# Performance work log

Hardware: AMD Instinct MI355X
Metric: run time of the kernel (lower is better)

Reference implementation:

```python
import jax, jax.numpy as jnp
import numpy as np

N, E = 50000, 1600000
NODE_F, EDGE_F = 128, 64
H, F = 4, 16
NEG_SLOPE = 0.2


def setup_inputs() -> dict:
    key = jax.random.key(0)
    ks = jax.random.split(key, 12)
    return {
        "nfeat": jax.random.normal(ks[0], (N, NODE_F), jnp.float32),
        "efeat": jax.random.normal(ks[1], (E, EDGE_F), jnp.float32),
        "W_node": jax.random.normal(ks[2], (NODE_F, H * F), jnp.float32) * 0.1,
        "b_node": jax.random.normal(ks[3], (H * F,), jnp.float32) * 0.1,
        "W_edge": jax.random.normal(ks[4], (EDGE_F, H * F), jnp.float32) * 0.1,
        "b_edge": jax.random.normal(ks[5], (H * F,), jnp.float32) * 0.1,
        "attn_l": jax.random.normal(ks[6], (H, F), jnp.float32) * 0.1,
        "attn_r": jax.random.normal(ks[7], (H, F), jnp.float32) * 0.1,
        "attn_e": jax.random.normal(ks[8], (H, F), jnp.float32) * 0.1,
        "src": jax.random.randint(ks[9], (E,), 0, N, jnp.int32),
        "dst": jax.random.randint(ks[10], (E,), 0, N, jnp.int32),
    }


def reference(nfeat, efeat, W_node, b_node, W_edge, b_edge,
              attn_l, attn_r, attn_e, src, dst):
    n = nfeat.shape[0]
    node_feat = (nfeat @ W_node + b_node).reshape(n, H, F)   # [N,H,F]
    edge_feat = (efeat @ W_edge + b_edge).reshape(-1, H, F)  # [E,H,F]
    el = jnp.einsum('nhf,hf->nh', node_feat, attn_l)  # [N,H]
    er = jnp.einsum('nhf,hf->nh', node_feat, attn_r)  # [N,H]
    ee = jnp.einsum('ehf,hf->eh', edge_feat, attn_e)  # [E,H]
    el_prime = el[src] + ee                            # u_add_e, [E,H]
    e = el_prime + er[dst]                             # e_add_v, [E,H]
    e = jnp.where(e > 0, e, NEG_SLOPE * e)             # leaky_relu
    # edge softmax over incoming edges per destination node
    emax = jax.ops.segment_max(e, dst, num_segments=n)      # [N,H]
    ex = jnp.exp(e - emax[dst])                              # [E,H]
    denom = jax.ops.segment_sum(ex, dst, num_segments=n)    # [N,H]
    a = ex / denom[dst]                                      # [E,H]
    # msg_fn: a * el_prime (scalar per edge/head) -> scatter-sum to dst
    m = a * el_prime                                          # [E,H]
    rst = jax.ops.segment_sum(m, dst, num_segments=n)        # [N,H]
    return rst[..., None]                                     # [N,H,1]
```

## Files before the change

kernel.cpp:

```cpp
#include <hip/hip_runtime.h>
#include <hip/hip_fp16.h>

constexpr int H = 4;
constexpr int F = 16;
constexpr int NODE_F = 128;
constexpr int EDGE_F = 64;
constexpr float NEG_SLOPE = 0.2f;

__global__ void node_proj_kernel(const float* __restrict__ nfeat,
                                 const float* __restrict__ Wn, const float* __restrict__ bn,
                                 const float* __restrict__ Wed, const float* __restrict__ bed,
                                 const float* __restrict__ al, const float* __restrict__ ar,
                                 const float* __restrict__ ae,
                                 float* __restrict__ el, float* __restrict__ er,
                                 float* __restrict__ Weg, float* __restrict__ beg,
                                 int* __restrict__ total, int* __restrict__ deg, int N) {
    __shared__ float sWl[NODE_F * H];
    __shared__ float sWr[NODE_F * H];
    __shared__ float sbl[H];
    __shared__ float sbr[H];
    for (int i = threadIdx.x; i < NODE_F * H; i += blockDim.x) {
        int k = i >> 2, h = i & 3;
        float sl = 0.f, sr = 0.f;
        #pragma unroll
        for (int f = 0; f < F; ++f) {
            float w = Wn[k * (H * F) + h * F + f];
            sl += w * al[h * F + f];
            sr += w * ar[h * F + f];
        }
        sWl[i] = sl; sWr[i] = sr;
    }
    if (threadIdx.x < H) {
        int h = threadIdx.x;
        float bl = 0.f, br = 0.f;
        #pragma unroll
        for (int f = 0; f < F; ++f) {
            bl += bn[h * F + f] * al[h * F + f];
            br += bn[h * F + f] * ar[h * F + f];
        }
        sbl[h] = bl; sbr[h] = br;
    }
    if (blockIdx.x == 0) {
        for (int i = threadIdx.x; i < EDGE_F * H; i += blockDim.x) {
            int k = i >> 2, h = i & 3;
            float s = 0.f;
            #pragma unroll
            for (int f = 0; f < F; ++f) s += Wed[k * (H * F) + h * F + f] * ae[h * F + f];
            Weg[i] = s;
        }
        if (threadIdx.x < H) {
            int h = threadIdx.x;
            float se = 0.f;
            #pragma unroll
            for (int f = 0; f < F; ++f) se += bed[h * F + f] * ae[h * F + f];
            beg[h] = se;
        }
        if (threadIdx.x == 0) *total = 0;
    }
    __syncthreads();
    int lane = threadIdx.x & 63;
    int wave = (int)(((size_t)blockIdx.x * blockDim.x + threadIdx.x) >> 6);
    int sub = lane & 3, ln = lane >> 2;
    int n = wave * 16 + ln;
    if (n >= N) return;
    float accl[H] = {0.f, 0.f, 0.f, 0.f};
    float accr[H] = {0.f, 0.f, 0.f, 0.f};
    const float4* row = (const float4*)(nfeat + (size_t)n * NODE_F);
    #pragma unroll
    for (int i = 0; i < 8; ++i) {
        float4 v = row[sub + 4 * i];
        int k0 = (sub + 4 * i) * 4;
        #pragma unroll
        for (int h = 0; h < H; ++h) {
            accl[h] += v.x * sWl[(k0 + 0) * H + h] + v.y * sWl[(k0 + 1) * H + h]
                     + v.z * sWl[(k0 + 2) * H + h] + v.w * sWl[(k0 + 3) * H + h];
            accr[h] += v.x * sWr[(k0 + 0) * H + h] + v.y * sWr[(k0 + 1) * H + h]
                     + v.z * sWr[(k0 + 2) * H + h] + v.w * sWr[(k0 + 3) * H + h];
        }
    }
    #pragma unroll
    for (int m = 1; m < 4; m <<= 1) {
        #pragma unroll
        for (int h = 0; h < H; ++h) {
            accl[h] += __shfl_xor(accl[h], m);
            accr[h] += __shfl_xor(accr[h], m);
        }
    }
    el[(size_t)n * H + sub] = accl[sub] + sbl[sub];
    er[(size_t)n * H + sub] = accr[sub] + sbr[sub];
    if (sub == 0) deg[n] = 0;
}

__global__ void edge_proj_kernel(const float* __restrict__ efeat,
                                 const int* __restrict__ src, const int* __restrict__ dst,
                                 const float* __restrict__ Weg, const float* __restrict__ beg,
                                 const float* __restrict__ el,
                                 uint2* __restrict__ pay, int* __restrict__ idx,
                                 int* __restrict__ deg, int E) {
    __shared__ float sWe[EDGE_F * H];
    __shared__ float sbe[H];
    for (int i = threadIdx.x; i < EDGE_F * H; i += blockDim.x) sWe[i] = Weg[i];
    if (threadIdx.x < H) sbe[threadIdx.x] = beg[threadIdx.x];
    __syncthreads();
    int lane = threadIdx.x & 63;
    int wave = (int)(((size_t)blockIdx.x * blockDim.x + threadIdx.x) >> 6);
    int sub = lane & 3, le = lane >> 2;
    int e = wave * 16 + le;
    if (e >= E) return;
    float acc[H] = {0.f, 0.f, 0.f, 0.f};
    const float4* row = (const float4*)(efeat + (size_t)e * EDGE_F);
    #pragma unroll
    for (int i = 0; i < 4; ++i) {
        float4 v = row[sub + 4 * i];
        int k0 = (sub + 4 * i) * 4;
        #pragma unroll
        for (int h = 0; h < H; ++h) {
            acc[h] += v.x * sWe[(k0 + 0) * H + h] + v.y * sWe[(k0 + 1) * H + h]
                    + v.z * sWe[(k0 + 2) * H + h] + v.w * sWe[(k0 + 3) * H + h];
        }
    }
    #pragma unroll
    for (int m = 1; m < 4; m <<= 1) {
        #pragma unroll
        for (int h = 0; h < H; ++h) acc[h] += __shfl_xor(acc[h], m);
    }
    if (sub == 0) {
        int s = src[e];
        float4 elv = *(const float4*)(el + (size_t)s * H);
        float p0 = elv.x + acc[0] + sbe[0];
        float p1 = elv.y + acc[1] + sbe[1];
        float p2 = elv.z + acc[2] + sbe[2];
        float p3 = elv.w + acc[3] + sbe[3];
        __half2 a = __floats2half2_rn(p0, p1);
        __half2 b = __floats2half2_rn(p2, p3);
        uint2 w;
        w.x = *(unsigned int*)&a;
        w.y = *(unsigned int*)&b;
        pay[e] = w;
        idx[e] = atomicAdd(deg + dst[e], 1);
    }
}

__global__ void offsets_kernel(const int* __restrict__ deg, int* __restrict__ off,
                               int* __restrict__ total, int N) {
    int lane = threadIdx.x & 63;
    int gid = blockIdx.x * blockDim.x + threadIdx.x;
    int x = (gid < N) ? deg[gid] : 0;
    int incl = x;
    #pragma unroll
    for (int s = 1; s < 64; s <<= 1) {
        int y = __shfl_up(incl, s);
        if (lane >= s) incl += y;
    }
    int wtot = __shfl(incl, 63);
    int base = 0;
    if (lane == 63) base = atomicAdd(total, wtot);
    base = __shfl(base, 63);
    if (gid < N) off[gid] = base + incl - x;
}

__global__ void scatter_eid_kernel(const int* __restrict__ dst, const int* __restrict__ idx,
                                   const int* __restrict__ off, int* __restrict__ eid, int E) {
    int e = blockIdx.x * blockDim.x + threadIdx.x;
    if (e >= E) return;
    __builtin_nontemporal_store(e, &eid[off[dst[e]] + idx[e]]);
}

__global__ void node_reduce_kernel(const uint2* __restrict__ pay,
                                   const int* __restrict__ eid,
                                   const int* __restrict__ off, const int* __restrict__ deg,
                                   const float* __restrict__ er,
                                   float* __restrict__ out, int N) {
    int lane = threadIdx.x & 63;
    int wave = (int)(((size_t)blockIdx.x * blockDim.x + threadIdx.x) >> 6);
    int g = lane >> 4;
    int gl = lane & 15;
    int n = wave * 4 + g;
    if (n >= N) return;
    int o = off[n], dg = deg[n];
    float4 erv = *(const float4*)(er + (size_t)n * H);
    float n0 = 0.f, n1 = 0.f, n2 = 0.f, n3 = 0.f;
    float d0 = 0.f, d1 = 0.f, d2 = 0.f, d3 = 0.f;
    for (int i = gl; i < dg; i += 16) {
        uint2 w = pay[eid[o + i]];
        float2 f01 = __half22float2(*(const __half2*)&w.x);
        float2 f23 = __half22float2(*(const __half2*)&w.y);
        float e0 = f01.x + erv.x, e1 = f01.y + erv.y, e2 = f23.x + erv.z, e3 = f23.y + erv.w;
        e0 = e0 > 0.f ? e0 : NEG_SLOPE * e0;
        e1 = e1 > 0.f ? e1 : NEG_SLOPE * e1;
        e2 = e2 > 0.f ? e2 : NEG_SLOPE * e2;
        e3 = e3 > 0.f ? e3 : NEG_SLOPE * e3;
        float x0 = expf(e0), x1 = expf(e1), x2 = expf(e2), x3 = expf(e3);
        n0 += x0 * f01.x; n1 += x1 * f01.y; n2 += x2 * f23.x; n3 += x3 * f23.y;
        d0 += x0; d1 += x1; d2 += x2; d3 += x3;
    }
    #pragma unroll
    for (int s = 8; s; s >>= 1) {
        n0 += __shfl_down(n0, s, 16); n1 += __shfl_down(n1, s, 16);
        n2 += __shfl_down(n2, s, 16); n3 += __shfl_down(n3, s, 16);
        d0 += __shfl_down(d0, s, 16); d1 += __shfl_down(d1, s, 16);
        d2 += __shfl_down(d2, s, 16); d3 += __shfl_down(d3, s, 16);
    }
    if (gl == 0) {
        *(float4*)(out + (size_t)n * H) =
            make_float4(d0 > 0.f ? n0 / d0 : 0.f, d1 > 0.f ? n1 / d1 : 0.f,
                        d2 > 0.f ? n2 / d2 : 0.f, d3 > 0.f ? n3 / d3 : 0.f);
    }
}

__global__ void fold_kernel(const float* __restrict__ Wn, const float* __restrict__ bn,
                            const float* __restrict__ Wed, const float* __restrict__ bed,
                            const float* __restrict__ al, const float* __restrict__ ar,
                            const float* __restrict__ ae,
                            float* __restrict__ Wl, float* __restrict__ Wr,
                            float* __restrict__ We, float* __restrict__ bv) {
    int idx = threadIdx.x;
    if (idx < NODE_F * H) {
        int k = idx >> 2, h = idx & 3;
        float sl = 0.f, sr = 0.f;
        #pragma unroll
        for (int f = 0; f < F; ++f) {
            float w = Wn[k * (H * F) + h * F + f];
            sl += w * al[h * F + f];
            sr += w * ar[h * F + f];
        }
        Wl[idx] = sl; Wr[idx] = sr;
    }
    if (idx < EDGE_F * H) {
        int k = idx >> 2, h = idx & 3;
        float s = 0.f;
        #pragma unroll
        for (int f = 0; f < F; ++f) s += Wed[k * (H * F) + h * F + f] * ae[h * F + f];
        We[idx] = s;
    }
    if (idx < H) {
        float sl = 0.f, sr = 0.f, se = 0.f;
        #pragma unroll
        for (int f = 0; f < F; ++f) {
            sl += bn[idx * F + f] * al[idx * F + f];
            sr += bn[idx * F + f] * ar[idx * F + f];
            se += bed[idx * F + f] * ae[idx * F + f];
        }
        bv[idx] = sl; bv[H + idx] = sr; bv[2 * H + idx] = se;
    }
}

__global__ void node_proj_fb_kernel(const float* __restrict__ nfeat,
                                    const float* __restrict__ Wl, const float* __restrict__ Wr,
                                    const float* __restrict__ bv,
                                    float* __restrict__ el, float* __restrict__ er,
                                    float* __restrict__ num, float* __restrict__ den, int N) {
    __shared__ float sWl[NODE_F * H];
    __shared__ float sWr[NODE_F * H];
    for (int i = threadIdx.x; i < NODE_F * H; i += blockDim.x) { sWl[i] = Wl[i]; sWr[i] = Wr[i]; }
    __syncthreads();
    int n = blockIdx.x * blockDim.x + threadIdx.x;
    if (n >= N) return;
    float accl[H] = {0.f, 0.f, 0.f, 0.f};
    float accr[H] = {0.f, 0.f, 0.f, 0.f};
    const float4* row = (const float4*)(nfeat + (size_t)n * NODE_F);
    #pragma unroll
    for (int j = 0; j < NODE_F / 4; ++j) {
        float4 v = row[j];
        #pragma unroll
        for (int h = 0; h < H; ++h) {
            accl[h] += v.x * sWl[(4 * j + 0) * H + h] + v.y * sWl[(4 * j + 1) * H + h]
                     + v.z * sWl[(4 * j + 2) * H + h] + v.w * sWl[(4 * j + 3) * H + h];
            accr[h] += v.x * sWr[(4 * j + 0) * H + h] + v.y * sWr[(4 * j + 1) * H + h]
                     + v.z * sWr[(4 * j + 2) * H + h] + v.w * sWr[(4 * j + 3) * H + h];
        }
    }
    size_t base = (size_t)n * H;
    #pragma unroll
    for (int h = 0; h < H; ++h) {
        el[base + h] = accl[h] + bv[h];
        er[base + h] = accr[h] + bv[H + h];
        num[base + h] = 0.f;
        den[base + h] = 0.f;
    }
}

__global__ void edge_atomic_kernel(const float* __restrict__ efeat,
                                   const int* __restrict__ src, const int* __restrict__ dst,
                                   const float* __restrict__ We, const float* __restrict__ bv,
                                   const float* __restrict__ el, const float* __restrict__ er,
                                   float* __restrict__ num, float* __restrict__ den, int E) {
    __shared__ float sWe[EDGE_F * H];
    __shared__ float sbe[H];
    for (int i = threadIdx.x; i < EDGE_F * H; i += blockDim.x) sWe[i] = We[i];
    if (threadIdx.x < H) sbe[threadIdx.x] = bv[2 * H + threadIdx.x];
    __syncthreads();
    int e = blockIdx.x * blockDim.x + threadIdx.x;
    if (e >= E) return;
    float acc[H] = {sbe[0], sbe[1], sbe[2], sbe[3]};
    const float4* row = (const float4*)(efeat + (size_t)e * EDGE_F);
    #pragma unroll
    for (int j = 0; j < EDGE_F / 4; ++j) {
        float4 v = row[j];
        #pragma unroll
        for (int h = 0; h < H; ++h) {
            acc[h] += v.x * sWe[(4 * j + 0) * H + h] + v.y * sWe[(4 * j + 1) * H + h]
                    + v.z * sWe[(4 * j + 2) * H + h] + v.w * sWe[(4 * j + 3) * H + h];
        }
    }
    int s = src[e], d = dst[e];
    float4 elv = *(const float4*)(el + (size_t)s * H);
    float4 erv = *(const float4*)(er + (size_t)d * H);
    float p0 = elv.x + acc[0], p1 = elv.y + acc[1], p2 = elv.z + acc[2], p3 = elv.w + acc[3];
    float e0 = p0 + erv.x, e1 = p1 + erv.y, e2 = p2 + erv.z, e3 = p3 + erv.w;
    e0 = e0 > 0.f ? e0 : NEG_SLOPE * e0;
    e1 = e1 > 0.f ? e1 : NEG_SLOPE * e1;
    e2 = e2 > 0.f ? e2 : NEG_SLOPE * e2;
    e3 = e3 > 0.f ? e3 : NEG_SLOPE * e3;
    float x0 = expf(e0), x1 = expf(e1), x2 = expf(e2), x3 = expf(e3);
    float* nb = num + (size_t)d * H;
    float* db = den + (size_t)d * H;
    atomicAdd(nb + 0, x0 * p0); atomicAdd(nb + 1, x1 * p1);
    atomicAdd(nb + 2, x2 * p2); atomicAdd(nb + 3, x3 * p3);
    atomicAdd(db + 0, x0); atomicAdd(db + 1, x1);
    atomicAdd(db + 2, x2); atomicAdd(db + 3, x3);
}

__global__ void finalize_kernel(const float* __restrict__ num, const float* __restrict__ den,
                                float* __restrict__ out, int NH) {
    int i = blockIdx.x * blockDim.x + threadIdx.x;
    if (i < NH) {
        float d = den[i];
        out[i] = d > 0.f ? num[i] / d : 0.f;
    }
}

extern "C" void kernel_launch(void* const* d_in, const int* in_sizes, int n_in,
                              void* d_out, int out_size, void* d_ws, size_t ws_size,
                              hipStream_t stream) {
    const float* nfeat = (const float*)d_in[0];
    const float* efeat = (const float*)d_in[1];
    const float* Wn    = (const float*)d_in[2];
    const float* bn    = (const float*)d_in[3];
    const float* Wed   = (const float*)d_in[4];
    const float* bed   = (const float*)d_in[5];
    const float* al    = (const float*)d_in[6];
    const float* ar    = (const float*)d_in[7];
    const float* ae    = (const float*)d_in[8];
    const int*   src   = (const int*)d_in[9];
    const int*   dst   = (const int*)d_in[10];

    int N = in_sizes[0] / NODE_F;
    int E = in_sizes[1] / EDGE_F;
    float* out = (float*)d_out;
    float* ws  = (float*)d_ws;

    size_t p_pay  = 0;
    size_t p_el   = p_pay + (size_t)E * 2;
    size_t p_er   = p_el + (size_t)N * H;
    size_t p_Weg  = p_er + (size_t)N * H;
    size_t p_beg  = p_Weg + 256;
    size_t p_tot  = p_beg + 16;
    size_t p_deg  = p_tot + 16;
    size_t p_off  = p_deg + (size_t)N;
    size_t p_idx  = p_off + (size_t)N;
    size_t p_eid  = p_idx + (size_t)E;
    size_t csr_total = (p_eid + (size_t)E) * sizeof(float);

    if (ws_size >= csr_total) {
        uint2* pay = (uint2*)(ws + p_pay);
        float* el  = ws + p_el;
        float* er  = ws + p_er;
        float* Weg = ws + p_Weg;
        float* beg = ws + p_beg;
        int* total = (int*)(ws + p_tot);
        int* deg   = (int*)(ws + p_deg);
        int* off   = (int*)(ws + p_off);
        int* idx   = (int*)(ws + p_idx);
        int* eid   = (int*)(ws + p_eid);

        node_proj_kernel<<<(int)(((size_t)N * 4 + 255) / 256), 256, 0, stream>>>(
            nfeat, Wn, bn, Wed, bed, al, ar, ae, el, er, Weg, beg, total, deg, N);
        edge_proj_kernel<<<(int)(((size_t)E * 4 + 255) / 256), 256, 0, stream>>>(
            efeat, src, dst, Weg, beg, el, pay, idx, deg, E);
        offsets_kernel<<<(N + 255) / 256, 256, 0, stream>>>(deg, off, total, N);
        scatter_eid_kernel<<<(E + 255) / 256, 256, 0, stream>>>(dst, idx, off, eid, E);
        node_reduce_kernel<<<(int)(((size_t)N * 16 + 255) / 256), 256, 0, stream>>>(
            pay, eid, off, deg, er, out, N);
    } else {
        float* el  = ws;
        float* er  = el + (size_t)N * H;
        float* num = er + (size_t)N * H;
        float* den = num + (size_t)N * H;
        float* Wl  = den + (size_t)N * H;
        float* Wr  = Wl + 512;
        float* We  = Wr + 512;
        float* bv  = We + 256;

        fold_kernel<<<1, 512, 0, stream>>>(Wn, bn, Wed, bed, al, ar, ae, Wl, Wr, We, bv);
        node_proj_fb_kernel<<<(N + 255) / 256, 256, 0, stream>>>(nfeat, Wl, Wr, bv,
                                                                 el, er, num, den, N);
        edge_atomic_kernel<<<(E + 255) / 256, 256, 0, stream>>>(efeat, src, dst, We, bv,
                                                                el, er, num, den, E);
        finalize_kernel<<<(N * H + 255) / 256, 256, 0, stream>>>(num, den, out, N * H);
    }
}
```

Measured before the change: 196.6 us.

## Hoist weight folding into one kernel, vectorize LDS reads, shrink idx to 16-bit

Moves the per-block folding of attention vectors into the weights out of node_proj into a single-block fold_kernel, so every node block now just copies the folded weights into shared memory. The node and edge projection inner loops read shared weights as float4 instead of scalar loads. The per-edge slot index becomes a 16-bit value to cut its write and read traffic, and the scatter uses a normal store instead of a nontemporal one. expf is replaced with the faster, less precise __expf. This adds one kernel launch, and the 16-bit index would overflow for any node whose in-degree exceeds 65535.

```diff
diff --git a/kernel.cpp b/kernel.cpp
--- a/kernel.cpp
+++ b/kernel.cpp
@@ -7,20 +7,17 @@
 constexpr int EDGE_F = 64;
 constexpr float NEG_SLOPE = 0.2f;
 
-__global__ void node_proj_kernel(const float* __restrict__ nfeat,
-                                 const float* __restrict__ Wn, const float* __restrict__ bn,
-                                 const float* __restrict__ Wed, const float* __restrict__ bed,
-                                 const float* __restrict__ al, const float* __restrict__ ar,
-                                 const float* __restrict__ ae,
-                                 float* __restrict__ el, float* __restrict__ er,
-                                 float* __restrict__ Weg, float* __restrict__ beg,
-                                 int* __restrict__ total, int* __restrict__ deg, int N) {
-    __shared__ float sWl[NODE_F * H];
-    __shared__ float sWr[NODE_F * H];
-    __shared__ float sbl[H];
-    __shared__ float sbr[H];
-    for (int i = threadIdx.x; i < NODE_F * H; i += blockDim.x) {
-        int k = i >> 2, h = i & 3;
+__global__ void fold_kernel(const float* __restrict__ Wn, const float* __restrict__ bn,
+                            const float* __restrict__ Wed, const float* __restrict__ bed,
+                            const float* __restrict__ al, const float* __restrict__ ar,
+                            const float* __restrict__ ae,
+                            float* __restrict__ Wl, float* __restrict__ Wr,
+                            float* __restrict__ We, float* __restrict__ bv,
+                            int* __restrict__ total) {
+    int idx = threadIdx.x;
+    if (idx == 0) *total = 0;
+    if (idx < NODE_F * H) {
+        int k = idx >> 2, h = idx & 3;
         float sl = 0.f, sr = 0.f;
         #pragma unroll
         for (int f = 0; f < F; ++f) {
@@ -28,35 +25,35 @@
             sl += w * al[h * F + f];
             sr += w * ar[h * F + f];
         }
-        sWl[i] = sl; sWr[i] = sr;
-    }
-    if (threadIdx.x < H) {
-        int h = threadIdx.x;
-        float bl = 0.f, br = 0.f;
+        Wl[idx] = sl; Wr[idx] = sr;
+    }
+    if (idx < EDGE_F * H) {
+        int k = idx >> 2, h = idx & 3;
+        float s = 0.f;
+        #pragma unroll
+        for (int f = 0; f < F; ++f) s += Wed[k * (H * F) + h * F + f] * ae[h * F + f];
+        We[idx] = s;
+    }
+    if (idx < H) {
+        float sl = 0.f, sr = 0.f, se = 0.f;
         #pragma unroll
         for (int f = 0; f < F; ++f) {
-            bl += bn[h * F + f] * al[h * F + f];
-            br += bn[h * F + f] * ar[h * F + f];
-        }
-        sbl[h] = bl; sbr[h] = br;
-    }
-    if (blockIdx.x == 0) {
-        for (int i = threadIdx.x; i < EDGE_F * H; i += blockDim.x) {
-            int k = i >> 2, h = i & 3;
-            float s = 0.f;
-            #pragma unroll
-            for (int f = 0; f < F; ++f) s += Wed[k * (H * F) + h * F + f] * ae[h * F + f];
-            Weg[i] = s;
-        }
-        if (threadIdx.x < H) {
-            int h = threadIdx.x;
-            float se = 0.f;
-            #pragma unroll
-            for (int f = 0; f < F; ++f) se += bed[h * F + f] * ae[h * F + f];
-            beg[h] = se;
-        }
-        if (threadIdx.x == 0) *total = 0;
-    }
+            sl += bn[idx * F + f] * al[idx * F + f];
+            sr += bn[idx * F + f] * ar[idx * F + f];
+            se += bed[idx * F + f] * ae[idx * F + f];
+        }
+        bv[idx] = sl; bv[H + idx] = sr; bv[2 * H + idx] = se;
+    }
+}
+
+__global__ void node_proj_kernel(const float* __restrict__ nfeat,
+                                 const float* __restrict__ Wl, const float* __restrict__ Wr,
+                                 const float* __restrict__ bv,
+                                 float* __restrict__ el, float* __restrict__ er,
+                                 int* __restrict__ deg, int N) {
+    __shared__ float sWl[NODE_F * H];
+    __shared__ float sWr[NODE_F * H];
+    for (int i = threadIdx.x; i < NODE_F * H; i += blockDim.x) { sWl[i] = Wl[i]; sWr[i] = Wr[i]; }
     __syncthreads();
     int lane = threadIdx.x & 63;
     int wave = (int)(((size_t)blockIdx.x * blockDim.x + threadIdx.x) >> 6);
@@ -70,12 +67,15 @@
     for (int i = 0; i < 8; ++i) {
         float4 v = row[sub + 4 * i];
         int k0 = (sub + 4 * i) * 4;
-        #pragma unroll
-        for (int h = 0; h < H; ++h) {
-            accl[h] += v.x * sWl[(k0 + 0) * H + h] + v.y * sWl[(k0 + 1) * H + h]
-                     + v.z * sWl[(k0 + 2) * H + h] + v.w * sWl[(k0 + 3) * H + h];
-            accr[h] += v.x * sWr[(k0 + 0) * H + h] + v.y * sWr[(k0 + 1) * H + h]
-                     + v.z * sWr[(k0 + 2) * H + h] + v.w * sWr[(k0 + 3) * H + h];
+        float vv[4] = {v.x, v.y, v.z, v.w};
+        #pragma unroll
+        for (int j = 0; j < 4; ++j) {
+            float4 wl = *(const float4*)&sWl[(k0 + j) * H];
+            float4 wr = *(const float4*)&sWr[(k0 + j) * H];
+            accl[0] += vv[j] * wl.x; accl[1] += vv[j] * wl.y;
+            accl[2] += vv[j] * wl.z; accl[3] += vv[j] * wl.w;
+            accr[0] += vv[j] * wr.x; accr[1] += vv[j] * wr.y;
+            accr[2] += vv[j] * wr.z; accr[3] += vv[j] * wr.w;
         }
     }
     #pragma unroll
@@ -86,21 +86,21 @@
             accr[h] += __shfl_xor(accr[h], m);
         }
     }
-    el[(size_t)n * H + sub] = accl[sub] + sbl[sub];
-    er[(size_t)n * H + sub] = accr[sub] + sbr[sub];
+    el[(size_t)n * H + sub] = accl[sub] + bv[sub];
+    er[(size_t)n * H + sub] = accr[sub] + bv[H + sub];
     if (sub == 0) deg[n] = 0;
 }
 
 __global__ void edge_proj_kernel(const float* __restrict__ efeat,
                                  const int* __restrict__ src, const int* __restrict__ dst,
-                                 const float* __restrict__ Weg, const float* __restrict__ beg,
+                                 const float* __restrict__ We, const float* __restrict__ bv,
                                  const float* __restrict__ el,
-                                 uint2* __restrict__ pay, int* __restrict__ idx,
+                                 uint2* __restrict__ pay, unsigned short* __restrict__ idx,
                                  int* __restrict__ deg, int E) {
     __shared__ float sWe[EDGE_F * H];
     __shared__ float sbe[H];
-    for (int i = threadIdx.x; i < EDGE_F * H; i += blockDim.x) sWe[i] = Weg[i];
-    if (threadIdx.x < H) sbe[threadIdx.x] = beg[threadIdx.x];
+    for (int i = threadIdx.x; i < EDGE_F * H; i += blockDim.x) sWe[i] = We[i];
+    if (threadIdx.x < H) sbe[threadIdx.x] = bv[2 * H + threadIdx.x];
     __syncthreads();
     int lane = threadIdx.x & 63;
     int wave = (int)(((size_t)blockIdx.x * blockDim.x + threadIdx.x) >> 6);
@@ -113,10 +113,12 @@
     for (int i = 0; i < 4; ++i) {
         float4 v = row[sub + 4 * i];
         int k0 = (sub + 4 * i) * 4;
-        #pragma unroll
-        for (int h = 0; h < H; ++h) {
-            acc[h] += v.x * sWe[(k0 + 0) * H + h] + v.y * sWe[(k0 + 1) * H + h]
-                    + v.z * sWe[(k0 + 2) * H + h] + v.w * sWe[(k0 + 3) * H + h];
+        float vv[4] = {v.x, v.y, v.z, v.w};
+        #pragma unroll
+        for (int j = 0; j < 4; ++j) {
+            float4 w = *(const float4*)&sWe[(k0 + j) * H];
+            acc[0] += vv[j] * w.x; acc[1] += vv[j] * w.y;
+            acc[2] += vv[j] * w.z; acc[3] += vv[j] * w.w;
         }
     }
     #pragma unroll
@@ -137,7 +139,7 @@
         w.x = *(unsigned int*)&a;
         w.y = *(unsigned int*)&b;
         pay[e] = w;
-        idx[e] = atomicAdd(deg + dst[e], 1);
+        idx[e] = (unsigned short)atomicAdd(deg + dst[e], 1);
     }
 }
 
@@ -159,11 +161,12 @@
     if (gid < N) off[gid] = base + incl - x;
 }
 
-__global__ void scatter_eid_kernel(const int* __restrict__ dst, const int* __restrict__ idx,
+__global__ void scatter_eid_kernel(const int* __restrict__ dst,
+                                   const unsigned short* __restrict__ idx,
                                    const int* __restrict__ off, int* __restrict__ eid, int E) {
     int e = blockIdx.x * blockDim.x + threadIdx.x;
     if (e >= E) return;
-    __builtin_nontemporal_store(e, &eid[off[dst[e]] + idx[e]]);
+    eid[off[dst[e]] + (int)idx[e]] = e;
 }
 
 __global__ void node_reduce_kernel(const uint2* __restrict__ pay,
@@ -190,7 +193,7 @@
         e1 = e1 > 0.f ? e1 : NEG_SLOPE * e1;
         e2 = e2 > 0.f ? e2 : NEG_SLOPE * e2;
         e3 = e3 > 0.f ? e3 : NEG_SLOPE * e3;
-        float x0 = expf(e0), x1 = expf(e1), x2 = expf(e2), x3 = expf(e3);
+        float x0 = __expf(e0), x1 = __expf(e1), x2 = __expf(e2), x3 = __expf(e3);
         n0 += x0 * f01.x; n1 += x1 * f01.y; n2 += x2 * f23.x; n3 += x3 * f23.y;
         d0 += x0; d1 += x1; d2 += x2; d3 += x3;
     }
@@ -205,43 +208,6 @@
         *(float4*)(out + (size_t)n * H) =
             make_float4(d0 > 0.f ? n0 / d0 : 0.f, d1 > 0.f ? n1 / d1 : 0.f,
                         d2 > 0.f ? n2 / d2 : 0.f, d3 > 0.f ? n3 / d3 : 0.f);
-    }
-}
-
-__global__ void fold_kernel(const float* __restrict__ Wn, const float* __restrict__ bn,
-                            const float* __restrict__ Wed, const float* __restrict__ bed,
-                            const float* __restrict__ al, const float* __restrict__ ar,
-                            const float* __restrict__ ae,
-                            float* __restrict__ Wl, float* __restrict__ Wr,
-                            float* __restrict__ We, float* __restrict__ bv) {
-    int idx = threadIdx.x;
-    if (idx < NODE_F * H) {
-        int k = idx >> 2, h = idx & 3;
-        float sl = 0.f, sr = 0.f;
-        #pragma unroll
-        for (int f = 0; f < F; ++f) {
-            float w = Wn[k * (H * F) + h * F + f];
-            sl += w * al[h * F + f];
-            sr += w * ar[h * F + f];
-        }
-        Wl[idx] = sl; Wr[idx] = sr;
-    }
-    if (idx < EDGE_F * H) {
-        int k = idx >> 2, h = idx & 3;
-        float s = 0.f;
-        #pragma unroll
-        for (int f = 0; f < F; ++f) s += Wed[k * (H * F) + h * F + f] * ae[h * F + f];
-        We[idx] = s;
-    }
-    if (idx < H) {
-        float sl = 0.f, sr = 0.f, se = 0.f;
-        #pragma unroll
-        for (int f = 0; f < F; ++f) {
-            sl += bn[idx * F + f] * al[idx * F + f];
-            sr += bn[idx * F + f] * ar[idx * F + f];
-            se += bed[idx * F + f] * ae[idx * F + f];
-        }
-        bv[idx] = sl; bv[H + idx] = sr; bv[2 * H + idx] = se;
     }
 }
 
@@ -312,7 +278,7 @@
     e1 = e1 > 0.f ? e1 : NEG_SLOPE * e1;
     e2 = e2 > 0.f ? e2 : NEG_SLOPE * e2;
     e3 = e3 > 0.f ? e3 : NEG_SLOPE * e3;
-    float x0 = expf(e0), x1 = expf(e1), x2 = expf(e2), x3 = expf(e3);
+    float x0 = __expf(e0), x1 = __expf(e1), x2 = __expf(e2), x3 = __expf(e3);
     float* nb = num + (size_t)d * H;
     float* db = den + (size_t)d * H;
     atomicAdd(nb + 0, x0 * p0); atomicAdd(nb + 1, x1 * p1);
@@ -353,31 +319,36 @@
     size_t p_pay  = 0;
     size_t p_el   = p_pay + (size_t)E * 2;
     size_t p_er   = p_el + (size_t)N * H;
-    size_t p_Weg  = p_er + (size_t)N * H;
-    size_t p_beg  = p_Weg + 256;
-    size_t p_tot  = p_beg + 16;
+    size_t p_Wl   = p_er + (size_t)N * H;
+    size_t p_Wr   = p_Wl + 512;
+    size_t p_We   = p_Wr + 512;
+    size_t p_bv   = p_We + 256;
+    size_t p_tot  = p_bv + 16;
     size_t p_deg  = p_tot + 16;
     size_t p_off  = p_deg + (size_t)N;
     size_t p_idx  = p_off + (size_t)N;
-    size_t p_eid  = p_idx + (size_t)E;
+    size_t p_eid  = p_idx + ((size_t)E / 2 + 8);
     size_t csr_total = (p_eid + (size_t)E) * sizeof(float);
 
     if (ws_size >= csr_total) {
         uint2* pay = (uint2*)(ws + p_pay);
         float* el  = ws + p_el;
         float* er  = ws + p_er;
-        float* Weg = ws + p_Weg;
-        float* beg = ws + p_beg;
+        float* Wl  = ws + p_Wl;
+        float* Wr  = ws + p_Wr;
+        float* We  = ws + p_We;
+        float* bv  = ws + p_bv;
         int* total = (int*)(ws + p_tot);
         int* deg   = (int*)(ws + p_deg);
         int* off   = (int*)(ws + p_off);
-        int* idx   = (int*)(ws + p_idx);
+        unsigned short* idx = (unsigned short*)(ws + p_idx);
         int* eid   = (int*)(ws + p_eid);
 
+        fold_kernel<<<1, 512, 0, stream>>>(Wn, bn, Wed, bed, al, ar, ae, Wl, Wr, We, bv, total);
         node_proj_kernel<<<(int)(((size_t)N * 4 + 255) / 256), 256, 0, stream>>>(
-            nfeat, Wn, bn, Wed, bed, al, ar, ae, el, er, Weg, beg, total, deg, N);
+            nfeat, Wl, Wr, bv, el, er, deg, N);
         edge_proj_kernel<<<(int)(((size_t)E * 4 + 255) / 256), 256, 0, stream>>>(
-            efeat, src, dst, Weg, beg, el, pay, idx, deg, E);
+            efeat, src, dst, We, bv, el, pay, idx, deg, E);
         offsets_kernel<<<(N + 255) / 256, 256, 0, stream>>>(deg, off, total, N);
         scatter_eid_kernel<<<(E + 255) / 256, 256, 0, stream>>>(dst, idx, off, eid, E);
         node_reduce_kernel<<<(int)(((size_t)N * 16 + 255) / 256), 256, 0, stream>>>(
@@ -391,8 +362,9 @@
         float* Wr  = Wl + 512;
         float* We  = Wr + 512;
         float* bv  = We + 256;
-
-        fold_kernel<<<1, 512, 0, stream>>>(Wn, bn, Wed, bed, al, ar, ae, Wl, Wr, We, bv);
+        int* total = (int*)(bv + 16);
+
+        fold_kernel<<<1, 512, 0, stream>>>(Wn, bn, Wed, bed, al, ar, ae, Wl, Wr, We, bv, total);
         node_proj_fb_kernel<<<(N + 255) / 256, 256, 0, stream>>>(nfeat, Wl, Wr, bv,
                                                                  el, er, num, den, N);
         edge_atomic_kernel<<<(E + 255) / 256, 256, 0, stream>>>(efeat, src, dst, We, bv,
```

After: 175.0 us. 1.12x faster.
